# Kernel optimization log

Hardware: AMD Instinct MI355X
Metric: run time of the kernel (lower is better)

The kernel has to match this reference:

```python
import jax, jax.numpy as jnp
import numpy as np

NX, NU, N, BATCH = 64, 32, 32, 192
NEWTON_ITERS = 2  # fixed outer Newton iterations (original loops to kkt_tol)


def setup_inputs() -> dict:
    key = jax.random.key(0)
    ks = jax.random.split(key, 8)
    x0 = jax.random.normal(ks[0], (BATCH, NX), jnp.float32)
    x = 0.1 * jax.random.normal(ks[1], (N + 1, BATCH, NX), jnp.float32)
    u = 0.1 * jax.random.normal(ks[2], (N, BATCH, NU), jnp.float32)
    lmd = jnp.zeros((N + 1, BATCH, NX), jnp.float32)
    # linear dynamics x+ = A x + Bm u (stable-ish A)
    A = 0.9 * jnp.eye(NX, dtype=jnp.float32) + (0.1 / np.sqrt(NX)) * jax.random.normal(ks[3], (NX, NX), jnp.float32)
    Bm = jax.random.normal(ks[4], (NX, NU), jnp.float32) / np.sqrt(NX)
    # quadratic cost weights (symmetric PD)
    Cx = jax.random.normal(ks[5], (NX, NX), jnp.float32) / np.sqrt(NX)
    Qx = Cx @ Cx.T + 0.1 * jnp.eye(NX, dtype=jnp.float32)
    Cu = jax.random.normal(ks[6], (NU, NU), jnp.float32) / np.sqrt(NU)
    Ru = Cu @ Cu.T + jnp.eye(NU, dtype=jnp.float32)
    Cf = jax.random.normal(ks[7], (NX, NX), jnp.float32) / np.sqrt(NX)
    Qf = Cf @ Cf.T + 0.1 * jnp.eye(NX, dtype=jnp.float32)
    return {"x0": x0, "x": x, "u": u, "lmd": lmd, "A": A, "Bm": Bm, "Qx": Qx, "Ru": Ru, "Qf": Qf}


def _eval_kkt(x0, x, u, lmd, A, Bm, Qx, Ru, Qf):
    # KKT residuals of the LQ OCP (GaussNewton; vectorized over stages s and batch b)
    x0res = x[0] - x0                                                   # [B,nx]
    xs = x[:-1]                                                         # [N,B,nx]
    xres = jnp.einsum('ij,sbj->sbi', A, xs) + jnp.einsum('ij,sbj->sbi', Bm, u) - x[1:]
    lx = jnp.einsum('ij,sbj->sbi', Qx, xs) + jnp.einsum('ji,sbj->sbi', A, lmd[1:]) - lmd[:-1]
    lu = jnp.einsum('ij,sbj->sbi', Ru, u) + jnp.einsum('ji,sbj->sbi', Bm, lmd[1:])
    lxN = jnp.einsum('ij,bj->bi', Qf, x[-1]) - lmd[-1]                  # terminal gradient residual
    return x0res, xres, lx, lu, lxN


def _riccati(x0res, xres, lx, lu, lxN, A, Bm, Qx, Ru, Qf):
    B_, nx = x0res.shape
    PN = jnp.broadcast_to(Qf, (B_, nx, nx))

    def bwd(carry, inp):
        P, p = carry
        lx_i, lu_i, xres_i = inp
        PA = jnp.einsum('bij,jk->bik', P, A)
        PB = jnp.einsum('bij,jk->bik', P, Bm)
        Qxx = Qx[None] + jnp.einsum('ji,bjk->bik', A, PA)
        Quu = Ru[None] + jnp.einsum('ji,bjk->bik', Bm, PB)
        Qxu = jnp.einsum('ji,bjk->bik', A, PB)
        w = jnp.einsum('bij,bj->bi', P, xres_i) + p
        qx = lx_i + jnp.einsum('ji,bj->bi', A, w)
        qu = lu_i + jnp.einsum('ji,bj->bi', Bm, w)
        rhs = jnp.concatenate([jnp.swapaxes(Qxu, 1, 2), qu[..., None]], axis=2)
        sol = -jnp.linalg.solve(Quu, rhs)
        K, k = sol[..., :nx], sol[..., nx]
        Pn = Qxx + jnp.einsum('bxi,biy->bxy', Qxu, K)
        Pn = 0.5 * (Pn + jnp.swapaxes(Pn, 1, 2))
        pn = qx + jnp.einsum('bxi,bi->bx', Qxu, k)
        return (Pn, pn), (Pn, pn, K, k)

    (_, _), (Ps, ps, Ks, ks) = jax.lax.scan(bwd, (PN, lxN), (lx, lu, xres), reverse=True)
    Ps = jnp.concatenate([Ps, PN[None]], axis=0)   # [N+1,B,nx,nx]
    ps = jnp.concatenate([ps, lxN[None]], axis=0)  # [N+1,B,nx]

    def fwd(dx, inp):
        K, k, xres_i = inp
        du = jnp.einsum('bux,bx->bu', K, dx) + k
        dxn = jnp.einsum('ij,bj->bi', A, dx) + jnp.einsum('ij,bj->bi', Bm, du) + xres_i
        return dxn, (dx, du)

    dxN, (dxs, dus) = jax.lax.scan(fwd, -x0res, (Ks, ks, xres))
    dxs = jnp.concatenate([dxs, dxN[None]], axis=0)
    dlmd = jnp.einsum('sbij,sbj->sbi', Ps, dxs) + ps
    return dxs, dus, dlmd


def _solve(x0, x, u, lmd, A, Bm, Qx, Ru, Qf):
    for _ in range(NEWTON_ITERS):
        x0res, xres, lx, lu, lxN = _eval_kkt(x0, x, u, lmd, A, Bm, Qx, Ru, Qf)
        dx, du, dlmd = _riccati(x0res, xres, lx, lu, lxN, A, Bm, Qx, Ru, Qf)
        x = x + dx
        u = u + du
        lmd = lmd + dlmd
    return x, u, lmd


def reference(x0, x, u, lmd, A, Bm, Qx, Ru, Qf):
    # returns the optimized control trajectory u* [N,B,nu]
    return _solve(x0, x, u, lmd, A, Bm, Qx, Ru, Qf)[1]
```

## Files before the change

### kernel.cpp

```cpp
#include <hip/hip_runtime.h>

#define DEV __device__ __forceinline__

constexpr int NX = 64, NU = 32, NH = 32, NB = 192;

constexpr int WS_P   = 0;
constexpr int WS_QI  = WS_P  + (NH + 1) * NX * NX;
constexpr int WS_X   = WS_QI + NH * NU * NU;
constexpr int WS_K   = WS_X  + NH * NX * NU;
constexpr int WS_STG = WS_K  + NH * NU * NX;

typedef __attribute__((ext_vector_type(8))) short bf16x8;
typedef __attribute__((ext_vector_type(4))) float f32x4;
typedef __attribute__((ext_vector_type(4))) unsigned short us4;

constexpr int LVL_M2T = 96 * 72 * 2;
constexpr int LVL_P   = 64 * 72 * 2;
constexpr int LVL_TT  = 96 * 72 * 2;
constexpr int LVL_XU  = 64 * 40 * 2;
constexpr int LVL_KT  = 64 * 40 * 2;
constexpr int LVL_QI  = 32 * 40 * 2;
constexpr int oM2T = 0;
constexpr int oP   = oM2T + 3 * LVL_M2T;
constexpr int oTT  = oP   + 3 * LVL_P;
constexpr int oXU  = oTT  + 3 * LVL_TT;
constexpr int oKT  = oXU  + 3 * LVL_XU;
constexpr int oQI  = oKT  + 3 * LVL_KT;
constexpr int oQUU = oQI  + 3 * LVL_QI;
constexpr int SMEMB = oQUU + 32 * 36 * 4;

DEV unsigned short bfh(float x) {
  unsigned u = __float_as_uint(x);
  return (unsigned short)((u + 0x7FFFu + ((u >> 16) & 1u)) >> 16);
}
DEV float bf2f(unsigned short h) { return __uint_as_float(((unsigned)h) << 16); }
DEV void split3(float x, unsigned short& h, unsigned short& m, unsigned short& l) {
  h = bfh(x); float r1 = x - bf2f(h);
  m = bfh(r1); float r2 = r1 - bf2f(m);
  l = bfh(r2);
}
DEV float4 ld4(const float* p) { return *reinterpret_cast<const float4*>(p); }
DEV void   st4(float* p, float4 v) { *reinterpret_cast<float4*>(p) = v; }
DEV void st4_nt(float* p, f32x4 v) {
  __builtin_nontemporal_store(v, (f32x4*)p);
}
DEV float  dot4(float4 a, float4 b) {
  return fmaf(a.x, b.x, fmaf(a.y, b.y, fmaf(a.z, b.z, a.w * b.w)));
}
DEV void fma4(float4& a, float s, float4 b) {
  a.x = fmaf(s, b.x, a.x); a.y = fmaf(s, b.y, a.y);
  a.z = fmaf(s, b.z, a.z); a.w = fmaf(s, b.w, a.w);
}
DEV void fma8(float* acc, float s, float4 b0, float4 b1) {
  acc[0] = fmaf(s, b0.x, acc[0]); acc[1] = fmaf(s, b0.y, acc[1]);
  acc[2] = fmaf(s, b0.z, acc[2]); acc[3] = fmaf(s, b0.w, acc[3]);
  acc[4] = fmaf(s, b1.x, acc[4]); acc[5] = fmaf(s, b1.y, acc[5]);
  acc[6] = fmaf(s, b1.z, acc[6]); acc[7] = fmaf(s, b1.w, acc[7]);
}

#define MFMA16(a, b, c) __builtin_amdgcn_mfma_f32_16x16x32_bf16(a, b, c, 0, 0, 0)

DEV f32x4 prod33(const char* A, int ao, int LA, const char* B, int bo, int LB,
                 f32x4 acc) {
  const bf16x8 a0 = *(const bf16x8*)(A + ao);
  const bf16x8 a1 = *(const bf16x8*)(A + LA + ao);
  const bf16x8 a2 = *(const bf16x8*)(A + 2 * LA + ao);
  const bf16x8 b0 = *(const bf16x8*)(B + bo);
  const bf16x8 b1 = *(const bf16x8*)(B + LB + bo);
  const bf16x8 b2 = *(const bf16x8*)(B + 2 * LB + bo);
  acc = MFMA16(a1, b1, acc);
  acc = MFMA16(a2, b0, acc);
  acc = MFMA16(a0, b2, acc);
  acc = MFMA16(a1, b0, acc);
  acc = MFMA16(a0, b1, acc);
  acc = MFMA16(a0, b0, acc);
  return acc;
}
DEV void st_pack3(char* base, int lvl, int el, f32x4 v) {
  us4 h, m, l;
#pragma unroll
  for (int r = 0; r < 4; ++r) {
    unsigned short hh, mm, ll; split3(v[r], hh, mm, ll);
    h[r] = (short)hh; m[r] = (short)mm; l[r] = (short)ll;
  }
  *(us4*)(base + el * 2) = h;
  *(us4*)(base + lvl + el * 2) = m;
  *(us4*)(base + 2 * lvl + el * 2) = l;
}

DEV void producer(char* smem, const float* Ag, const float* Bg,
                  const float* Qxg, const float* Rug, const float* Qfg,
                  float* ws) {
  const int t = threadIdx.x, lane = t & 63, wv = t >> 6;
  const int l15 = lane & 15, l4 = lane >> 4;

  char* M2T = smem + oM2T;
  char* Pp  = smem + oP;
  char* TT  = smem + oTT;
  char* XU  = smem + oXU;
  char* KT  = smem + oKT;
  char* QI  = smem + oQI;
  float* QUU = (float*)(smem + oQUU);

  float* gP   = ws + WS_P;
  float* gQI  = ws + WS_QI;
  float* gX   = ws + WS_X;
  float* gK   = ws + WS_K;
  float* gStg = ws + WS_STG;
  int* flags  = (int*)(ws + WS_P);

  for (int idx = t; idx < 96 * 64; idx += 512) {
    const int j = idx >> 6, m = idx & 63;
    const float v = (j < 64) ? Ag[m * 64 + j] : Bg[m * 32 + (j - 64)];
    unsigned short h, mi, lo; split3(v, h, mi, lo);
    const int eo = (j * 72 + m) * 2;
    *(unsigned short*)(M2T + eo) = h;
    *(unsigned short*)(M2T + LVL_M2T + eo) = mi;
    *(unsigned short*)(M2T + 2 * LVL_M2T + eo) = lo;
  }
  for (int idx = t; idx < 64 * 64; idx += 512) {
    const int r = idx >> 6, c = idx & 63;
    const float v = Qfg[idx];
    unsigned short h, mi, lo; split3(v, h, mi, lo);
    const int eo = (r * 72 + c) * 2;
    *(unsigned short*)(Pp + eo) = h;
    *(unsigned short*)(Pp + LVL_P + eo) = mi;
    *(unsigned short*)(Pp + 2 * LVL_P + eo) = lo;
    __builtin_nontemporal_store(v, gP + 32 * 4096 + idx);
  }
  __syncthreads();

  for (int s = NH - 1; s >= 0; --s) {
#pragma unroll
    for (int q = 0; q < 3; ++q) {
      const int tt = wv + q * 8;
      const int isV = tt >= 16;
      const int t2 = isV ? tt - 16 : tt;
      const int mT = t2 & 3;
      const int br = (isV ? 64 : 0) + (t2 >> 2) * 16;
      f32x4 acc = {0.f, 0.f, 0.f, 0.f};
#pragma unroll
      for (int kp = 0; kp < 2; ++kp) {
        const int ao = ((mT * 16 + l15) * 72 + kp * 32 + l4 * 8) * 2;
        const int bo = ((br + l15) * 72 + kp * 32 + l4 * 8) * 2;
        acc = prod33(Pp, ao, LVL_P, M2T, bo, LVL_M2T, acc);
      }
      st_pack3(TT, LVL_TT, (br + l15) * 72 + mT * 16 + l4 * 4, acc);
    }
    __syncthreads();

    if (wv < 4) {
      const int uA = wv >> 1, uB = wv & 1;
      f32x4 acc = {0.f, 0.f, 0.f, 0.f};
#pragma unroll
      for (int kp = 0; kp < 2; ++kp) {
        const int ao = ((64 + uA * 16 + l15) * 72 + kp * 32 + l4 * 8) * 2;
        const int bo = ((64 + uB * 16 + l15) * 72 + kp * 32 + l4 * 8) * 2;
        acc = prod33(TT, ao, LVL_TT, M2T, bo, LVL_M2T, acc);
      }
      const int c = uB * 16 + l15, u0 = uA * 16 + l4 * 4;
      const float4 rv = ld4(Rug + c * 32 + u0);
      QUU[c * 36 + u0 + 0] = acc[0] + rv.x;
      QUU[c * 36 + u0 + 1] = acc[1] + rv.y;
      QUU[c * 36 + u0 + 2] = acc[2] + rv.z;
      QUU[c * 36 + u0 + 3] = acc[3] + rv.w;
    } else {
#pragma unroll
      for (int q = 0; q < 2; ++q) {
        const int tt = (wv - 4) * 2 + q;
        const int uT = tt & 1, xT = tt >> 1;
        f32x4 acc = {0.f, 0.f, 0.f, 0.f};
#pragma unroll
        for (int kp = 0; kp < 2; ++kp) {
          const int ao = ((64 + uT * 16 + l15) * 72 + kp * 32 + l4 * 8) * 2;
          const int bo = ((xT * 16 + l15) * 72 + kp * 32 + l4 * 8) * 2;
          acc = prod33(TT, ao, LVL_TT, M2T, bo, LVL_M2T, acc);
        }
        const int x = xT * 16 + l15, u0 = uT * 16 + l4 * 4;
        st_pack3(XU, LVL_XU, x * 40 + u0, acc);
        st4_nt(gX + s * 2048 + x * 32 + u0, acc);
      }
    }
    __syncthreads();

    if (wv == 0) {
      const int i = lane & 31, h = lane >> 5;
      float W[16];
#pragma unroll
      for (int r = 0; r < 16; ++r) W[r] = QUU[i * 36 + h * 16 + r];
#pragma unroll
      for (int j = 0; j < 32; ++j) {
        const int jh = j >> 4, jr = j & 15;
        const float d = __shfl(W[jr], j | (jh << 5));
        const float pinv = 1.0f / d;
        const float f = __shfl(W[jr], i | (jh << 5));
        float pr[16];
#pragma unroll
        for (int r = 0; r < 16; ++r) pr[r] = __shfl(W[r], j | (h << 5));
        float nw[16];
        if (i == j) {
#pragma unroll
          for (int r = 0; r < 16; ++r) nw[r] = pr[r] * pinv;
          if (h == jh) nw[jr] = pinv;
        } else {
          const float g = f * pinv;
#pragma unroll
          for (int r = 0; r < 16; ++r) nw[r] = fmaf(-g, pr[r], W[r]);
          if (h == jh) nw[jr] = -g;
        }
#pragma unroll
        for (int r = 0; r < 16; ++r) W[r] = nw[r];
      }
#pragma unroll
      for (int q = 0; q < 4; ++q) {
        f32x4 o = {W[4 * q], W[4 * q + 1], W[4 * q + 2], W[4 * q + 3]};
        st4_nt(gQI + s * 1024 + i * 32 + h * 16 + 4 * q, o);
        st_pack3(QI, LVL_QI, i * 40 + h * 16 + 4 * q, o);
      }
    } else {
#pragma unroll
      for (int q = 0; q < 3; ++q) {
        const int tt = (wv - 1) + q * 7;
        if (tt < 16) {
          const int jT = tt >> 2, iT = tt & 3;
          f32x4 acc = {0.f, 0.f, 0.f, 0.f};
#pragma unroll
          for (int kp = 0; kp < 2; ++kp) {
            const int ao = ((jT * 16 + l15) * 72 + kp * 32 + l4 * 8) * 2;
            const int bo = ((iT * 16 + l15) * 72 + kp * 32 + l4 * 8) * 2;
            acc = prod33(TT, ao, LVL_TT, M2T, bo, LVL_M2T, acc);
          }
          const int c = iT * 16 + l15, j0 = jT * 16 + l4 * 4;
          const float4 qv = ld4(Qxg + c * 64 + j0);
          float4 o; o.x = acc[0] + qv.x; o.y = acc[1] + qv.y;
          o.z = acc[2] + qv.z; o.w = acc[3] + qv.w;
          st4(gStg + c * 64 + j0, o);
        }
      }
    }
    __syncthreads();

    {
      const int mT = wv & 1, xT = wv >> 1;
      f32x4 acc = {0.f, 0.f, 0.f, 0.f};
      const int ao = ((mT * 16 + l15) * 40 + l4 * 8) * 2;
      const int bo = ((xT * 16 + l15) * 40 + l4 * 8) * 2;
      acc = prod33(QI, ao, LVL_QI, XU, bo, LVL_XU, acc);
      const int x = xT * 16 + l15, m0 = mT * 16 + l4 * 4;
#pragma unroll
      for (int r = 0; r < 4; ++r)
        __builtin_nontemporal_store(-acc[r], gK + s * 2048 + (m0 + r) * 64 + x);
      st_pack3(KT, LVL_KT, x * 40 + m0, acc);
    }
    __syncthreads();

    if (t == 0)
      __hip_atomic_store(flags + s, 1, __ATOMIC_RELEASE, __HIP_MEMORY_SCOPE_AGENT);

    if (s > 0) {
#pragma unroll
      for (int q = 0; q < 2; ++q) {
        const int tt = wv + q * 8;
        const int iT = tt & 3, jT = tt >> 2;
        f32x4 acc = {0.f, 0.f, 0.f, 0.f};
        const int ao = ((iT * 16 + l15) * 40 + l4 * 8) * 2;
        const int bo = ((jT * 16 + l15) * 40 + l4 * 8) * 2;
        acc = prod33(XU, ao, LVL_XU, KT, bo, LVL_KT, acc);
        const int j = jT * 16 + l15, i0 = iT * 16 + l4 * 4;
        const float4 qx4 = ld4(gStg + j * 64 + i0);
        f32x4 pv;
        pv[0] = qx4.x - acc[0]; pv[1] = qx4.y - acc[1];
        pv[2] = qx4.z - acc[2]; pv[3] = qx4.w - acc[3];
#pragma unroll
        for (int r = 0; r < 4; ++r)
          __builtin_nontemporal_store(pv[r], gP + s * 4096 + (i0 + r) * 64 + j);
        st_pack3(Pp, LVL_P, j * 72 + i0, pv);
      }
    }
    __syncthreads();
  }
}

DEV void consumer(float* lds, int b, const float* x0g, const float* xg,
                  const float* ug, const float* lg, const float* Ag,
                  const float* Bg, const float* Qxg, const float* Rug,
                  const float* Qfg, float* ws, float* outp) {
  const int t = threadIdx.x;
  const float* gP  = ws + WS_P;
  const float* gQI = ws + WS_QI;
  const float* gX  = ws + WS_X;
  const float* gK  = ws + WS_K;
  int* flags = (int*)(ws + WS_P);

  float* sx   = lds;
  float* sl   = lds + 2112;
  float* su   = lds + 4224;
  float* sAT  = lds;
  float* xres = lds + 5248;
  float* lxs  = lds + 7296;
  float* lus  = lds + 9344;
  float* kv   = lds + 10368;
  float* swv  = lds + 11392;
  float* sqv  = lds + 11456;
  float* sduv = lds + 11488;
  float* sdxv = lds + 11520;

  for (int idx = t; idx < (NH + 1) * NX; idx += 512) {
    const int s = idx >> 6, i = idx & 63;
    sx[idx] = xg[(s * NB + b) * NX + i];
    sl[idx] = lg[(s * NB + b) * NX + i];
  }
  for (int idx = t; idx < NH * NU; idx += 512) {
    const int s = idx >> 5, j = idx & 31;
    su[idx] = ug[(s * NB + b) * NU + j];
  }
  __syncthreads();

  if (t < 256) {
    const int s = t >> 3, i0 = (t & 7) * 8;
    float accx[8], accl[8];
#pragma unroll
    for (int ii = 0; ii < 8; ++ii) {
      accx[ii] = -sx[(s + 1) * NX + i0 + ii];
      accl[ii] = -sl[s * NX + i0 + ii];
    }
#pragma unroll 2
    for (int k0 = 0; k0 < NX; k0 += 4) {
      const float4 xv = ld4(sx + s * NX + k0);
#pragma unroll
      for (int ii = 0; ii < 8; ++ii) {
        accx[ii] += dot4(ld4(Ag + (i0 + ii) * NX + k0), xv);
        accl[ii] += dot4(ld4(Qxg + (i0 + ii) * NX + k0), xv);
      }
    }
#pragma unroll 2
    for (int k0 = 0; k0 < NU; k0 += 4) {
      const float4 uv = ld4(su + s * NU + k0);
#pragma unroll
      for (int ii = 0; ii < 8; ++ii)
        accx[ii] += dot4(ld4(Bg + (i0 + ii) * NU + k0), uv);
    }
#pragma unroll 4
    for (int k = 0; k < NX; ++k) {
      const float lv = sl[(s + 1) * NX + k];
      fma8(accl, lv, ld4(Ag + k * NX + i0), ld4(Ag + k * NX + i0 + 4));
    }
#pragma unroll
    for (int ii = 0; ii < 8; ++ii) {
      xres[s * NX + i0 + ii] = accx[ii];
      lxs[s * NX + i0 + ii] = accl[ii];
    }
  }
  if (t < 256) {
    const int s = t >> 3, j0 = (t & 7) * 4;
    float4 acc = {0, 0, 0, 0};
#pragma unroll 2
    for (int k0 = 0; k0 < NU; k0 += 4) {
      const float4 uv = ld4(su + s * NU + k0);
      acc.x += dot4(ld4(Rug + (j0 + 0) * NU + k0), uv);
      acc.y += dot4(ld4(Rug + (j0 + 1) * NU + k0), uv);
      acc.z += dot4(ld4(Rug + (j0 + 2) * NU + k0), uv);
      acc.w += dot4(ld4(Rug + (j0 + 3) * NU + k0), uv);
    }
#pragma unroll 4
    for (int k = 0; k < NX; ++k) {
      const float lv = sl[(s + 1) * NX + k];
      fma4(acc, lv, ld4(Bg + k * NU + j0));
    }
    lus[s * NU + j0 + 0] = acc.x; lus[s * NU + j0 + 1] = acc.y;
    lus[s * NU + j0 + 2] = acc.z; lus[s * NU + j0 + 3] = acc.w;
  }

  float p_i = 0.0f, dx_i = 0.0f;
  if (t < 64) {
    const int i = t;
    float acc = -sl[NH * NX + i];
#pragma unroll 4
    for (int k0 = 0; k0 < NX; k0 += 4)
      acc += dot4(ld4(Qfg + i * NX + k0), ld4(sx + NH * NX + k0));
    p_i = acc;
    dx_i = x0g[b * NX + i] - sx[i];
  }
  __syncthreads();

  for (int idx = t; idx < NX * NX / 4; idx += 512) {
    const int k = idx >> 4, i4 = (idx & 15) * 4;
    const float4 a4 = ld4(Ag + k * NX + i4);
    sAT[(i4 + 0) * 68 + k] = a4.x;
    sAT[(i4 + 1) * 68 + k] = a4.y;
    sAT[(i4 + 2) * 68 + k] = a4.z;
    sAT[(i4 + 3) * 68 + k] = a4.w;
  }
  __syncthreads();

  if (t >= 64) return;

  const int i = t;
  const int j = t & 31;
  const int hh = t >> 5;

  for (int s = NH - 1; s >= 0; --s) {
    while (__hip_atomic_load(flags + s, __ATOMIC_RELAXED,
                             __HIP_MEMORY_SCOPE_AGENT) == 0)
      __builtin_amdgcn_s_sleep(4);
    (void)__hip_atomic_load(flags + s, __ATOMIC_ACQUIRE,
                            __HIP_MEMORY_SCOPE_AGENT);

    const float* Pr = gP + (s + 1) * NX * NX + i * NX;
    const float* xr = xres + s * NX;
    float w = p_i;
#pragma unroll
    for (int k0 = 0; k0 < NX; k0 += 16) {
      w += dot4(ld4(Pr + k0),      ld4(xr + k0));
      w += dot4(ld4(Pr + k0 + 4),  ld4(xr + k0 + 4));
      w += dot4(ld4(Pr + k0 + 8),  ld4(xr + k0 + 8));
      w += dot4(ld4(Pr + k0 + 12), ld4(xr + k0 + 12));
    }
    swv[i] = w;

    float qx = lxs[s * NX + i];
#pragma unroll
    for (int k0 = 0; k0 < NX; k0 += 16) {
      qx += dot4(ld4(sAT + i * 68 + k0),      ld4(swv + k0));
      qx += dot4(ld4(sAT + i * 68 + k0 + 4),  ld4(swv + k0 + 4));
      qx += dot4(ld4(sAT + i * 68 + k0 + 8),  ld4(swv + k0 + 8));
      qx += dot4(ld4(sAT + i * 68 + k0 + 12), ld4(swv + k0 + 12));
    }

    float qa = 0.0f;
    const int kb = hh * 32;
#pragma unroll 8
    for (int kk = 0; kk < 32; ++kk)
      qa = fmaf(Bg[(kb + kk) * NU + j], swv[kb + kk], qa);
    qa += __shfl_xor(qa, 32);
    const float qu = qa + lus[s * NU + j];
    if (hh == 0) sqv[j] = qu;

    const float* Qr = gQI + s * NU * NU + j * NU + hh * 16;
    float ka = dot4(ld4(Qr),      ld4(sqv + hh * 16))
             + dot4(ld4(Qr + 4),  ld4(sqv + hh * 16 + 4))
             + dot4(ld4(Qr + 8),  ld4(sqv + hh * 16 + 8))
             + dot4(ld4(Qr + 12), ld4(sqv + hh * 16 + 12));
    ka += __shfl_xor(ka, 32);
    if (hh == 0) kv[s * NU + j] = -ka;

    const float* Xs = gX + s * 2048 + i * 32;
    float pp = qx;
#pragma unroll
    for (int m0 = 0; m0 < NU; m0 += 4)
      pp += dot4(ld4(Xs + m0), ld4(kv + s * NU + m0));
    p_i = pp;
  }

  sdxv[i] = dx_i;
  for (int s = 0; s < NH; ++s) {
    const float* Kr = gK + s * NU * NX + j * NX + hh * 32;
    const float* dxh = sdxv + hh * 32;
    float da = 0.0f;
#pragma unroll
    for (int k0 = 0; k0 < 32; k0 += 16) {
      da += dot4(ld4(Kr + k0),      ld4(dxh + k0));
      da += dot4(ld4(Kr + k0 + 4),  ld4(dxh + k0 + 4));
      da += dot4(ld4(Kr + k0 + 8),  ld4(dxh + k0 + 8));
      da += dot4(ld4(Kr + k0 + 12), ld4(dxh + k0 + 12));
    }
    da += __shfl_xor(da, 32);
    const float du = da + kv[s * NU + j];
    if (hh == 0) {
      const int gi = (s * NB + b) * NU + j;
      outp[gi] = ug[gi] + du;
      sduv[j] = du;
    }

    float nxv = xres[s * NX + i];
    const float* Ar = Ag + i * NX;
#pragma unroll
    for (int k0 = 0; k0 < NX; k0 += 4)
      nxv += dot4(ld4(Ar + k0), ld4(sdxv + k0));
    const float* Br = Bg + i * NU;
#pragma unroll
    for (int m0 = 0; m0 < NU; m0 += 4)
      nxv += dot4(ld4(Br + m0), ld4(sduv + m0));
    sdxv[i] = nxv;
  }
}

__global__ void k_zero(float* ws) {
  if (threadIdx.x < 64) ((int*)(ws + WS_P))[threadIdx.x] = 0;
}

__global__ __launch_bounds__(512) void k_fused(
    const float* __restrict__ x0g, const float* __restrict__ xg,
    const float* __restrict__ ug, const float* __restrict__ lg,
    const float* __restrict__ Ag, const float* __restrict__ Bg,
    const float* __restrict__ Qxg, const float* __restrict__ Rug,
    const float* __restrict__ Qfg, float* __restrict__ ws,
    float* __restrict__ outp) {
  __shared__ __align__(16) char smem[SMEMB];
  if (blockIdx.x == 0)
    producer(smem, Ag, Bg, Qxg, Rug, Qfg, ws);
  else
    consumer((float*)smem, blockIdx.x - 1, x0g, xg, ug, lg, Ag, Bg, Qxg, Rug,
             Qfg, ws, outp);
}

extern "C" void kernel_launch(void* const* d_in, const int* in_sizes, int n_in,
                              void* d_out, int out_size, void* d_ws, size_t ws_size,
                              hipStream_t stream) {
  const float* x0  = (const float*)d_in[0];
  const float* x   = (const float*)d_in[1];
  const float* u   = (const float*)d_in[2];
  const float* lmd = (const float*)d_in[3];
  const float* A   = (const float*)d_in[4];
  const float* Bm  = (const float*)d_in[5];
  const float* Qx  = (const float*)d_in[6];
  const float* Ru  = (const float*)d_in[7];
  const float* Qf  = (const float*)d_in[8];
  float* ws  = (float*)d_ws;
  float* out = (float*)d_out;

  hipLaunchKernelGGL(k_zero, dim3(1), dim3(64), 0, stream, ws);
  hipLaunchKernelGGL(k_fused, dim3(NB + 1), dim3(512), 0, stream,
                     x0, x, u, lmd, A, Bm, Qx, Ru, Qf, ws, out);
}
```

Before: 418.0 us.

## Block 2x2 pivot Gauss-Jordan, regular stores, and prefetch gains in consumer loops

The producer's 32x32 Gauss-Jordan inversion now eliminates two pivots per step using a 2x2 block inverse, halving the serial pivot chain. Nontemporal stores of P, X, K and Qinv are replaced with regular stores, and a threadfence is added before the release flag. Consumer blocks prefetch X and Qinv rows right after the flag wait and double-buffer K rows in the forward pass to hide global load latency. The 2x2 pivoting assumes the leading 2x2 blocks stay well conditioned, which holds for SPD Quu but changes rounding slightly.

```diff
diff --git a/kernel.cpp b/kernel.cpp
--- a/kernel.cpp
+++ b/kernel.cpp
@@ -41,9 +41,7 @@
 }
 DEV float4 ld4(const float* p) { return *reinterpret_cast<const float4*>(p); }
 DEV void   st4(float* p, float4 v) { *reinterpret_cast<float4*>(p) = v; }
-DEV void st4_nt(float* p, f32x4 v) {
-  __builtin_nontemporal_store(v, (f32x4*)p);
-}
+DEV void   st4v(float* p, f32x4 v) { *reinterpret_cast<f32x4*>(p) = v; }
 DEV float  dot4(float4 a, float4 b) {
   return fmaf(a.x, b.x, fmaf(a.y, b.y, fmaf(a.z, b.z, a.w * b.w)));
 }
@@ -126,7 +124,7 @@
     *(unsigned short*)(Pp + eo) = h;
     *(unsigned short*)(Pp + LVL_P + eo) = mi;
     *(unsigned short*)(Pp + 2 * LVL_P + eo) = lo;
-    __builtin_nontemporal_store(v, gP + 32 * 4096 + idx);
+    gP[32 * 4096 + idx] = v;
   }
   __syncthreads();
 
@@ -178,7 +176,7 @@
         }
         const int x = xT * 16 + l15, u0 = uT * 16 + l4 * 4;
         st_pack3(XU, LVL_XU, x * 40 + u0, acc);
-        st4_nt(gX + s * 2048 + x * 32 + u0, acc);
+        st4v(gX + s * 2048 + x * 32 + u0, acc);
       }
     }
     __syncthreads();
@@ -189,24 +187,40 @@
 #pragma unroll
       for (int r = 0; r < 16; ++r) W[r] = QUU[i * 36 + h * 16 + r];
 #pragma unroll
-      for (int j = 0; j < 32; ++j) {
-        const int jh = j >> 4, jr = j & 15;
-        const float d = __shfl(W[jr], j | (jh << 5));
-        const float pinv = 1.0f / d;
-        const float f = __shfl(W[jr], i | (jh << 5));
-        float pr[16];
-#pragma unroll
-        for (int r = 0; r < 16; ++r) pr[r] = __shfl(W[r], j | (h << 5));
+      for (int q = 0; q < 16; ++q) {
+        const int p0 = 2 * q, p1 = 2 * q + 1;
+        const int jh = p0 >> 4, jr0 = p0 & 15, jr1 = jr0 + 1;
+        const float a = __shfl(W[jr0], p0 | (jh << 5));
+        const float b = __shfl(W[jr1], p0 | (jh << 5));
+        const float c = __shfl(W[jr0], p1 | (jh << 5));
+        const float d = __shfl(W[jr1], p1 | (jh << 5));
+        const float rdet = 1.0f / fmaf(a, d, -b * c);
+        const float Di00 = d * rdet, Di01 = -b * rdet;
+        const float Di10 = -c * rdet, Di11 = a * rdet;
+        const float f0 = __shfl(W[jr0], i | (jh << 5));
+        const float f1 = __shfl(W[jr1], i | (jh << 5));
+        float pr0[16], pr1[16];
+#pragma unroll
+        for (int r = 0; r < 16; ++r) {
+          pr0[r] = __shfl(W[r], p0 | (h << 5));
+          pr1[r] = __shfl(W[r], p1 | (h << 5));
+        }
+        const float g0 = fmaf(f0, Di00, f1 * Di10);
+        const float g1 = fmaf(f0, Di01, f1 * Di11);
         float nw[16];
-        if (i == j) {
-#pragma unroll
-          for (int r = 0; r < 16; ++r) nw[r] = pr[r] * pinv;
-          if (h == jh) nw[jr] = pinv;
+        if (i == p0) {
+#pragma unroll
+          for (int r = 0; r < 16; ++r) nw[r] = fmaf(Di00, pr0[r], Di01 * pr1[r]);
+          if (h == jh) { nw[jr0] = Di00; nw[jr1] = Di01; }
+        } else if (i == p1) {
+#pragma unroll
+          for (int r = 0; r < 16; ++r) nw[r] = fmaf(Di10, pr0[r], Di11 * pr1[r]);
+          if (h == jh) { nw[jr0] = Di10; nw[jr1] = Di11; }
         } else {
-          const float g = f * pinv;
-#pragma unroll
-          for (int r = 0; r < 16; ++r) nw[r] = fmaf(-g, pr[r], W[r]);
-          if (h == jh) nw[jr] = -g;
+#pragma unroll
+          for (int r = 0; r < 16; ++r)
+            nw[r] = fmaf(-g0, pr0[r], fmaf(-g1, pr1[r], W[r]));
+          if (h == jh) { nw[jr0] = -g0; nw[jr1] = -g1; }
         }
 #pragma unroll
         for (int r = 0; r < 16; ++r) W[r] = nw[r];
@@ -214,7 +228,7 @@
 #pragma unroll
       for (int q = 0; q < 4; ++q) {
         f32x4 o = {W[4 * q], W[4 * q + 1], W[4 * q + 2], W[4 * q + 3]};
-        st4_nt(gQI + s * 1024 + i * 32 + h * 16 + 4 * q, o);
+        st4v(gQI + s * 1024 + i * 32 + h * 16 + 4 * q, o);
         st_pack3(QI, LVL_QI, i * 40 + h * 16 + 4 * q, o);
       }
     } else {
@@ -249,13 +263,15 @@
       const int x = xT * 16 + l15, m0 = mT * 16 + l4 * 4;
 #pragma unroll
       for (int r = 0; r < 4; ++r)
-        __builtin_nontemporal_store(-acc[r], gK + s * 2048 + (m0 + r) * 64 + x);
+        gK[s * 2048 + (m0 + r) * 64 + x] = -acc[r];
       st_pack3(KT, LVL_KT, x * 40 + m0, acc);
     }
     __syncthreads();
 
-    if (t == 0)
+    if (t == 0) {
+      __threadfence();
       __hip_atomic_store(flags + s, 1, __ATOMIC_RELEASE, __HIP_MEMORY_SCOPE_AGENT);
+    }
 
     if (s > 0) {
 #pragma unroll
@@ -273,7 +289,7 @@
         pv[2] = qx4.z - acc[2]; pv[3] = qx4.w - acc[3];
 #pragma unroll
         for (int r = 0; r < 4; ++r)
-          __builtin_nontemporal_store(pv[r], gP + s * 4096 + (i0 + r) * 64 + j);
+          gP[s * 4096 + (i0 + r) * 64 + j] = pv[r];
         st_pack3(Pp, LVL_P, j * 72 + i0, pv);
       }
     }
@@ -406,6 +422,19 @@
     (void)__hip_atomic_load(flags + s, __ATOMIC_ACQUIRE,
                             __HIP_MEMORY_SCOPE_AGENT);
 
+    float4 xpre[8];
+    {
+      const float* Xs = gX + s * 2048 + i * 32;
+#pragma unroll
+      for (int q = 0; q < 8; ++q) xpre[q] = ld4(Xs + q * 4);
+    }
+    float4 qipre[4];
+    {
+      const float* Qr = gQI + s * NU * NU + j * NU + hh * 16;
+#pragma unroll
+      for (int q = 0; q < 4; ++q) qipre[q] = ld4(Qr + q * 4);
+    }
+
     const float* Pr = gP + (s + 1) * NX * NX + i * NX;
     const float* xr = xres + s * NX;
     float w = p_i;
@@ -436,34 +465,40 @@
     const float qu = qa + lus[s * NU + j];
     if (hh == 0) sqv[j] = qu;
 
-    const float* Qr = gQI + s * NU * NU + j * NU + hh * 16;
-    float ka = dot4(ld4(Qr),      ld4(sqv + hh * 16))
-             + dot4(ld4(Qr + 4),  ld4(sqv + hh * 16 + 4))
-             + dot4(ld4(Qr + 8),  ld4(sqv + hh * 16 + 8))
-             + dot4(ld4(Qr + 12), ld4(sqv + hh * 16 + 12));
+    float ka = dot4(qipre[0], ld4(sqv + hh * 16))
+             + dot4(qipre[1], ld4(sqv + hh * 16 + 4))
+             + dot4(qipre[2], ld4(sqv + hh * 16 + 8))
+             + dot4(qipre[3], ld4(sqv + hh * 16 + 12));
     ka += __shfl_xor(ka, 32);
     if (hh == 0) kv[s * NU + j] = -ka;
 
-    const float* Xs = gX + s * 2048 + i * 32;
     float pp = qx;
 #pragma unroll
-    for (int m0 = 0; m0 < NU; m0 += 4)
-      pp += dot4(ld4(Xs + m0), ld4(kv + s * NU + m0));
+    for (int m0 = 0; m0 < 8; ++m0)
+      pp += dot4(xpre[m0], ld4(kv + s * NU + m0 * 4));
     p_i = pp;
   }
 
   sdxv[i] = dx_i;
+  float4 kcur[8];
+  {
+    const float* Kr = gK + j * NX + hh * 32;
+#pragma unroll
+    for (int q = 0; q < 8; ++q) kcur[q] = ld4(Kr + q * 4);
+  }
   for (int s = 0; s < NH; ++s) {
-    const float* Kr = gK + s * NU * NX + j * NX + hh * 32;
     const float* dxh = sdxv + hh * 32;
     float da = 0.0f;
 #pragma unroll
-    for (int k0 = 0; k0 < 32; k0 += 16) {
-      da += dot4(ld4(Kr + k0),      ld4(dxh + k0));
-      da += dot4(ld4(Kr + k0 + 4),  ld4(dxh + k0 + 4));
-      da += dot4(ld4(Kr + k0 + 8),  ld4(dxh + k0 + 8));
-      da += dot4(ld4(Kr + k0 + 12), ld4(dxh + k0 + 12));
-    }
+    for (int q = 0; q < 8; ++q) da += dot4(kcur[q], ld4(dxh + q * 4));
+
+    float4 knxt[8];
+    if (s + 1 < NH) {
+      const float* Kn = gK + (s + 1) * 2048 + j * NX + hh * 32;
+#pragma unroll
+      for (int q = 0; q < 8; ++q) knxt[q] = ld4(Kn + q * 4);
+    }
+
     da += __shfl_xor(da, 32);
     const float du = da + kv[s * NU + j];
     if (hh == 0) {
@@ -482,6 +517,11 @@
     for (int m0 = 0; m0 < NU; m0 += 4)
       nxv += dot4(ld4(Br + m0), ld4(sduv + m0));
     sdxv[i] = nxv;
+
+    if (s + 1 < NH) {
+#pragma unroll
+      for (int q = 0; q < 8; ++q) kcur[q] = knxt[q];
+    }
   }
 }
 
```

Measured after the change: 458.4 us. 1.1x slower.
